# Performance work log

Measured on AMD Instinct MI355X. Metric: run time of the kernel, lower is better.

The kernel has to match this reference:

```python
import jax, jax.numpy as jnp
import numpy as np

BATCH = 65536
VEC = 512       # CLIP embedding dim
K = 1024        # num_cluster
GAMMA = 0.99
EPS = 1e-05


def setup_inputs() -> dict:
    key = jax.random.key(0)
    k1, k2, k3 = jax.random.split(key, 3)
    batch_vectors = jax.random.normal(k1, (BATCH, VEC), dtype=jnp.float32)
    weight = jax.random.normal(k2, (VEC, K), dtype=jnp.float32)        # codebook, stored (vec_size, num_cluster)
    cluster_size = jnp.ones((K,), dtype=jnp.float32)
    embed_avg = jax.random.normal(k3, (VEC, K), dtype=jnp.float32)
    return {
        "batch_vectors": batch_vectors,
        "weight": weight,
        "cluster_size": cluster_size,
        "embed_avg": embed_avg,
    }


def reference(batch_vectors, weight, cluster_size, embed_avg):
    """One minibatch_update step of clusteringEMA_torch.

    Returns the updated codebook `weight` of shape (vec_size, num_cluster).
    """
    gamma = GAMMA
    eps = EPS
    num_cluster = weight.shape[1]

    # nearest centroid: squared L2 distance has the same argmin as the L2 norm
    x2 = jnp.sum(batch_vectors * batch_vectors, axis=1, keepdims=True)   # (B,1)
    w2 = jnp.sum(weight * weight, axis=0)[None, :]                       # (1,K)
    dist2 = x2 + w2 - 2.0 * (batch_vectors @ weight)                     # (B,K)
    argmin = jnp.argmin(dist2, axis=-1)                                  # (B,)

    # per-cluster counts (one-hot sum), zeros replaced by 1
    counts = jnp.zeros((num_cluster,), dtype=batch_vectors.dtype).at[argmin].add(1.0)
    n_idx_choice = jnp.where(counts == 0, 1.0, counts)

    # EMA of cluster sizes
    new_cluster_size = gamma * cluster_size + (1.0 - gamma) * n_idx_choice

    # embed_sum = x^T @ onehot  == per-cluster sum of assigned vectors, (vec,K)
    embed_sum = jax.ops.segment_sum(batch_vectors, argmin, num_segments=num_cluster).T
    new_embed_avg = gamma * embed_avg + (1.0 - gamma) * embed_sum

    # Laplace-smoothed normalization
    n = jnp.sum(new_cluster_size)
    cs = (new_cluster_size + eps) / (n + num_cluster * eps) * n
    new_weight = new_embed_avg / cs[None, :]
    return new_weight
```

## Files before the change

kernel.cpp:

```cpp
#include <hip/hip_runtime.h>

typedef unsigned int uint;
typedef unsigned short ushort_t;
typedef unsigned long long u64;
typedef __attribute__((ext_vector_type(4))) float f32x4;
typedef __attribute__((ext_vector_type(8))) __bf16 bf16x8;
typedef __attribute__((ext_vector_type(8))) unsigned short us8;

#define BATCH 65536
#define VEC 512
#define K 1024
#define GAMMA 0.99f
#define EPS 1e-05f
#define SEG 64
#define MARGIN 0.75f

#define NKT (VEC / 32)

__device__ __forceinline__ ushort_t rtn(float f) {
    uint u = __float_as_uint(f);
    return (ushort_t)((u + 0x7FFFu + ((u >> 16) & 1u)) >> 16);
}

__device__ __forceinline__ void gl16(const void* g, void* l) {
    __builtin_amdgcn_global_load_lds(
        (const __attribute__((address_space(1))) unsigned int*)g,
        (__attribute__((address_space(3))) unsigned int*)l, 16, 0, 0);
}

__device__ __forceinline__ float dec_key(uint e) {
    uint b = (e & 0x80000000u) ? (e & 0x7FFFFFFFu) : ~e;
    return __uint_as_float(b);
}

__global__ void k_pack_w(const float* __restrict__ w, us8* __restrict__ wpk,
                         float* __restrict__ wT, float* __restrict__ w2p,
                         int* __restrict__ cc ) {
    __shared__ float lds[32][257];
    const int g = blockIdx.x;
    const int gx = g >> 4, ks = g & 15;
    const int t = threadIdx.x;

#pragma unroll
    for (int r = 0; r < 32; ++r)
        lds[r][t] = w[(size_t)(ks * 32 + r) * K + gx * 256 + t];
    __syncthreads();

    float s = 0.f;
#pragma unroll
    for (int r = 0; r < 32; ++r) { float f = lds[r][t]; s += f * f; }
    w2p[ks * K + gx * 256 + t] = s;

#pragma unroll
    for (int i = 0; i < 4; ++i) {
        const int o = i * 256 + t;
        const int lane = o & 63, ct = o >> 6;
        const int cl = ct * 16 + (lane & 15);
        const int r0 = (lane >> 4) * 8;
        us8 v;
#pragma unroll
        for (int j = 0; j < 8; ++j) v[j] = rtn(lds[r0 + j][cl]);
        wpk[(size_t)g * 1024 + o] = v;
    }

#pragma unroll
    for (int rr = 0; rr < 8; ++rr) {
        f32x4 v = {lds[rr * 4 + 0][t], lds[rr * 4 + 1][t], lds[rr * 4 + 2][t], lds[rr * 4 + 3][t]};
        *(f32x4*)&wT[(size_t)(gx * 256 + t) * VEC + ks * 32 + rr * 4] = v;
    }

    if (g < 8) cc[g * 256 + t] = 0;
    if (g == 8 && t == 0) cc[2048] = 0;
}

__launch_bounds__(512, 4)
__global__ void k_gemm(const float* __restrict__ x, const us8* __restrict__ wpk,
                       const float* __restrict__ w2p,
                       u64* __restrict__ keysA, u64* __restrict__ keysB) {
    __shared__ us8 a_lds[2][512];
    __shared__ us8 b_lds[2][1024];

    const int blk = blockIdx.x;
    const int gy = (blk & 7) * 64 + ((blk >> 3) >> 2);
    const int gx = (blk >> 3) & 3;
    const int t = threadIdx.x;
    const int lane = t & 63;
    const int wv = t >> 6;
    const int wm = wv >> 2;
    const int wn = wv & 3;

    const us8* bsrc = wpk + (size_t)gx * (NKT * 1024);

    const int al = t & 63;
    const float* xp = x + (size_t)(gy * 128 + (t >> 6) * 16 + (al & 15)) * VEC + (al >> 4) * 8;
    f32x4 av0, av1;
    auto aload = [&](int kt) {
        const float* p = xp + kt * 32;
        av0 = *(const f32x4*)p;
        av1 = *(const f32x4*)(p + 4);
    };
    auto awrite = [&](int buf) {
        us8 h;
#pragma unroll
        for (int j = 0; j < 4; ++j) { h[j] = rtn(av0[j]); h[4 + j] = rtn(av1[j]); }
        a_lds[buf][t] = h;
    };
    auto bstage = [&](int buf, int kt) {
        const us8* sb = bsrc + (size_t)kt * 1024;
        gl16(sb + t, &b_lds[buf][t]);
        gl16(sb + 512 + t, &b_lds[buf][512 + t]);
    };

    f32x4 acc[4][4];
#pragma unroll
    for (int i = 0; i < 4; ++i)
#pragma unroll
        for (int j = 0; j < 4; ++j) acc[i][j] = (f32x4){0.f, 0.f, 0.f, 0.f};

    aload(0);
    bstage(0, 0);
    awrite(0);
    __syncthreads();

    for (int tk = 0; tk < NKT; ++tk) {
        const int buf = tk & 1;
        const bool nx = (tk + 1 < NKT);
        if (nx) {
            aload(tk + 1);
            bstage(buf ^ 1, tk + 1);
        }
        bf16x8 bh[4];
#pragma unroll
        for (int ct = 0; ct < 4; ++ct)
            bh[ct] = __builtin_bit_cast(bf16x8, b_lds[buf][(wn * 4 + ct) * 64 + lane]);
#pragma unroll
        for (int rt = 0; rt < 4; ++rt) {
            bf16x8 ah = __builtin_bit_cast(bf16x8, a_lds[buf][(wm * 4 + rt) * 64 + lane]);
#pragma unroll
            for (int ct = 0; ct < 4; ++ct)
                acc[rt][ct] = __builtin_amdgcn_mfma_f32_16x16x32_bf16(ah, bh[ct], acc[rt][ct], 0, 0, 0);
        }
        if (nx) awrite(buf ^ 1);
        __syncthreads();
    }

    const int col_base = gx * 256 + wn * 64;
    float w2c[4];
#pragma unroll
    for (int ct = 0; ct < 4; ++ct) {
        const int col = col_base + ct * 16 + (lane & 15);
        float s = 0.f;
#pragma unroll
        for (int p = 0; p < 16; ++p) s += w2p[p * K + col];
        w2c[ct] = s;
    }
    const int slot = gx * 4 + wn;

#pragma unroll
    for (int rt = 0; rt < 4; ++rt) {
#pragma unroll
        for (int reg = 0; reg < 4; ++reg) {
            u64 k1 = ~0ull, k2 = ~0ull;
#pragma unroll
            for (int ct = 0; ct < 4; ++ct) {
                float dist = w2c[ct] - 2.0f * acc[rt][ct][reg];
                uint su = __float_as_uint(dist);
                su = (su & 0x80000000u) ? ~su : (su | 0x80000000u);
                const u64 key = ((u64)su << 32) | (uint)(col_base + ct * 16 + (lane & 15));
                if (key < k1) { k2 = k1; k1 = key; }
                else if (key < k2) { k2 = key; }
            }
#pragma unroll
            for (int m = 1; m < 16; m <<= 1) {
                u64 o1 = __shfl_xor((unsigned long long)k1, m);
                u64 o2 = __shfl_xor((unsigned long long)k2, m);
                u64 lo = k1 < o1 ? k1 : o1;
                u64 hi = k1 < o1 ? o1 : k1;
                u64 mn2 = k2 < o2 ? k2 : o2;
                k1 = lo;
                k2 = hi < mn2 ? hi : mn2;
            }
            if ((lane & 15) == 0) {
                const int row = gy * 128 + wm * 64 + rt * 16 + (lane >> 4) * 4 + reg;
                keysA[(size_t)slot * BATCH + row] = k1;
                keysB[(size_t)slot * BATCH + row] = k2;
            }
        }
    }
}

__global__ void k_verify(const u64* __restrict__ keysA, const u64* __restrict__ keysB,
                         int* __restrict__ am, int* __restrict__ counts,
                         u64* __restrict__ list, int* __restrict__ listcnt,
                         float* __restrict__ esum) {
    const int r = blockIdx.x * 256 + threadIdx.x;
    f32x4 z = {0.f, 0.f, 0.f, 0.f};
    ((f32x4*)esum)[r * 2] = z;
    ((f32x4*)esum)[r * 2 + 1] = z;

    u64 m1 = ~0ull, s = ~0ull;
    int i1 = 0;
#pragma unroll
    for (int i = 0; i < 16; ++i) {
        u64 a = keysA[(size_t)i * BATCH + r];
        if (a < m1) { s = m1; m1 = a; i1 = i; }
        else if (a < s) s = a;
    }
    u64 b = keysB[(size_t)i1 * BATCH + r];
    u64 m2 = s < b ? s : b;

    const float d1 = dec_key((uint)(m1 >> 32));
    const float d2 = dec_key((uint)(m2 >> 32));
    const int c1 = (int)(uint)m1 & 1023;
    const int c2 = (int)(uint)m2 & 1023;

    if (d2 - d1 > MARGIN) {
        am[r] = c1;
        atomicAdd(&counts[c1], 1);
    } else {
        int p = atomicAdd(listcnt, 1);
        list[p] = ((u64)(uint)r << 32) | ((uint)c1 << 10) | (uint)c2;
    }
}

__launch_bounds__(256)
__global__ void k_recheck(const float* __restrict__ x, const float* __restrict__ wT,
                          const float* __restrict__ w2p, const u64* __restrict__ list,
                          const int* __restrict__ listcnt, int* __restrict__ am,
                          int* __restrict__ counts) {
    const int gwid = (blockIdx.x * 256 + threadIdx.x) >> 6;
    const int lane = threadIdx.x & 63;
    const int n = *listcnt;
    for (int idx = gwid; idx < n; idx += 1024) {
        const u64 e = list[idx];
        const int r = (int)(e >> 32);
        const int c1 = (int)((e >> 10) & 1023);
        const int c2 = (int)(e & 1023);
        const f32x4 x0 = *(const f32x4*)&x[(size_t)r * VEC + lane * 8];
        const f32x4 x1 = *(const f32x4*)&x[(size_t)r * VEC + lane * 8 + 4];
        float d[2];
        const int cc[2] = {c1, c2};
#pragma unroll
        for (int j = 0; j < 2; ++j) {
            const int c = cc[j];
            const f32x4 w0 = *(const f32x4*)&wT[(size_t)c * VEC + lane * 8];
            const f32x4 w1 = *(const f32x4*)&wT[(size_t)c * VEC + lane * 8 + 4];
            float p = x0[0] * w0[0] + x0[1] * w0[1] + x0[2] * w0[2] + x0[3] * w0[3]
                    + x1[0] * w1[0] + x1[1] * w1[1] + x1[2] * w1[2] + x1[3] * w1[3];
#pragma unroll
            for (int m = 1; m < 64; m <<= 1) p += __shfl_xor(p, m);
            float w2 = 0.f;
#pragma unroll
            for (int q = 0; q < 16; ++q) w2 += w2p[q * K + c];
            d[j] = w2 - 2.0f * p;
        }
        const int win = (d[0] < d[1] || (d[0] == d[1] && c1 < c2)) ? c1 : c2;
        if (lane == 0) {
            am[r] = win;
            atomicAdd(&counts[win], 1);
        }
    }
}

__global__ void k_scan(const int* __restrict__ counts,
                       const float* __restrict__ cluster_size,
                       int* __restrict__ offsets, float* __restrict__ cs) {
    __shared__ int wsum[16];
    __shared__ float fw[16];
    const int t = threadIdx.x;
    const int lane = t & 63, wid = t >> 6;
    const int c = counts[t];

    int s = c;
#pragma unroll
    for (int d = 1; d < 64; d <<= 1) {
        int o = __shfl_up(s, d);
        if (lane >= d) s += o;
    }
    float ncs = GAMMA * cluster_size[t] + (1.0f - GAMMA) * ((c == 0) ? 1.0f : (float)c);
    float fs = ncs;
#pragma unroll
    for (int d = 32; d > 0; d >>= 1) fs += __shfl_xor(fs, d);

    if (lane == 63) wsum[wid] = s;
    if (lane == 0) fw[wid] = fs;
    __syncthreads();
    if (wid == 0 && lane < 16) {
        int v = wsum[lane];
#pragma unroll
        for (int d = 1; d < 16; d <<= 1) {
            int o = __shfl_up(v, d);
            if (lane >= d) v += o;
        }
        wsum[lane] = v;
    }
    __syncthreads();
    const int base = wid ? wsum[wid - 1] : 0;
    offsets[t] = base + s - c;

    float n = 0.f;
#pragma unroll
    for (int i = 0; i < 16; ++i) n += fw[i];
    cs[t] = (ncs + EPS) / (n + (float)K * EPS) * n;
}

__global__ void k_scatter(const int* __restrict__ am, const int* __restrict__ offsets,
                          int* __restrict__ cursor, int* __restrict__ sorted,
                          int* __restrict__ sortedk) {
    const int b = blockIdx.x * blockDim.x + threadIdx.x;
    const int k = am[b];
    const int pos = atomicAdd(&cursor[k], 1);
    sorted[offsets[k] + pos] = b;
    sortedk[offsets[k] + pos] = k;
}

__launch_bounds__(512)
__global__ void k_segred(const float* __restrict__ x, const int* __restrict__ sorted,
                         const int* __restrict__ sortedk, float* __restrict__ esum) {
    __shared__ int srow[SEG];
    __shared__ int skid[SEG];
    const int b = blockIdx.x;
    const int t = threadIdx.x;
    if (t < SEG) {
        srow[t] = sorted[b * SEG + t];
        skid[t] = sortedk[b * SEG + t];
    }
    __syncthreads();

    float a = 0.f;
    int cur = skid[0];
#pragma unroll 8
    for (int i = 0; i < SEG; ++i) {
        const int k = skid[i];
        if (k != cur) {
            atomicAdd(&esum[(size_t)cur * VEC + t], a);
            a = 0.f;
            cur = k;
        }
        a += x[(size_t)srow[i] * VEC + t];
    }
    atomicAdd(&esum[(size_t)cur * VEC + t], a);
}

__launch_bounds__(256)
__global__ void k_finalize(const float* __restrict__ esum, const float* __restrict__ embed_avg,
                           const float* __restrict__ cs, float* __restrict__ out) {
    __shared__ float tile[64][65];
    const int k0 = blockIdx.x * 64;
    const int v0 = blockIdx.y * 64;
    const int c = threadIdx.x & 63;
    const int r0 = threadIdx.x >> 6;
#pragma unroll
    for (int j = 0; j < 16; ++j) {
        const int r = r0 + j * 4;
        tile[r][c] = esum[(size_t)(k0 + r) * VEC + v0 + c];
    }
    __syncthreads();
    const float csk = cs[k0 + c];
#pragma unroll
    for (int j = 0; j < 16; ++j) {
        const int r = r0 + j * 4;
        const size_t o = (size_t)(v0 + r) * K + k0 + c;
        out[o] = (GAMMA * embed_avg[o] + (1.0f - GAMMA) * tile[c][r]) / csk;
    }
}

extern "C" void kernel_launch(void* const* d_in, const int* in_sizes, int n_in,
                              void* d_out, int out_size, void* d_ws, size_t ws_size,
                              hipStream_t stream) {
    const float* x            = (const float*)d_in[0];
    const float* w            = (const float*)d_in[1];
    const float* cluster_size = (const float*)d_in[2];
    const float* embed_avg    = (const float*)d_in[3];
    float* out = (float*)d_out;

    u64*   keysA   = (u64*)d_ws;
    u64*   keysB   = keysA + (size_t)16 * BATCH;
    int*   am      = (int*)(keysB + (size_t)16 * BATCH);
    u64*   list    = (u64*)(am + BATCH);
    float* w2p     = (float*)(list + BATCH);
    float* cs      = w2p + 16 * K;
    int*   cc      = (int*)(cs + K);
    int*   counts  = cc;
    int*   cursor  = cc + K;
    int*   listcnt = cc + 2 * K;
    int*   offsets = cc + 2 * K + 64;
    int*   sorted  = offsets + K;
    int*   sortedk = sorted + BATCH;
    float* esum    = (float*)(sortedk + BATCH);
    us8*   wpk     = (us8*)(esum + (size_t)K * VEC);
    float* wT      = (float*)(wpk + (size_t)64 * 1024);

    k_pack_w<<<64, 256, 0, stream>>>(w, wpk, wT, w2p, cc);
    k_gemm<<<2048, 512, 0, stream>>>(x, wpk, w2p, keysA, keysB);
    k_verify<<<BATCH / 256, 256, 0, stream>>>(keysA, keysB, am, counts, list, listcnt, esum);
    k_recheck<<<256, 256, 0, stream>>>(x, wT, w2p, list, listcnt, am, counts);
    k_scan<<<1, K, 0, stream>>>(counts, cluster_size, offsets, cs);
    k_scatter<<<BATCH / 256, 256, 0, stream>>>(am, offsets, cursor, sorted, sortedk);
    k_segred<<<BATCH / SEG, 512, 0, stream>>>(x, sorted, sortedk, esum);
    k_finalize<<<dim3(K / 64, VEC / 64), 256, 0, stream>>>(esum, embed_avg, cs, out);
}
```

Measured before the change: 388.0 us.

## Enlarge GEMM tile to 256 rows with K-step 64 and vectorize segment reduction

Each GEMM block now covers 256 rows instead of 128 and steps through K in chunks of 64, with each wave holding 8x4 accumulator tiles. This doubles reuse of every B fragment across row tiles and halves the number of barriers and K iterations. The weight packing kernel is reworked to match the new layout, and the partial norm array shrinks to 8 slices. The cost is more registers and LDS per block, lowering occupancy to 2 blocks per CU. The segment reduction now has threads load float4 values over strided rows, which creates more atomic operations per thread.

```diff
diff --git a/kernel.cpp b/kernel.cpp
--- a/kernel.cpp
+++ b/kernel.cpp
@@ -15,7 +15,7 @@
 #define SEG 64
 #define MARGIN 0.75f
 
-#define NKT (VEC / 32)
+#define NKT (VEC / 64)
 
 __device__ __forceinline__ ushort_t rtn(float f) {
     uint u = __float_as_uint(f);
@@ -38,82 +38,95 @@
                          int* __restrict__ cc ) {
     __shared__ float lds[32][257];
     const int g = blockIdx.x;
-    const int gx = g >> 4, ks = g & 15;
+    const int gx = g >> 3, tk = g & 7;
     const int t = threadIdx.x;
 
-#pragma unroll
-    for (int r = 0; r < 32; ++r)
-        lds[r][t] = w[(size_t)(ks * 32 + r) * K + gx * 256 + t];
-    __syncthreads();
-
     float s = 0.f;
 #pragma unroll
-    for (int r = 0; r < 32; ++r) { float f = lds[r][t]; s += f * f; }
-    w2p[ks * K + gx * 256 + t] = s;
-
-#pragma unroll
-    for (int i = 0; i < 4; ++i) {
-        const int o = i * 256 + t;
-        const int lane = o & 63, ct = o >> 6;
-        const int cl = ct * 16 + (lane & 15);
-        const int r0 = (lane >> 4) * 8;
-        us8 v;
-#pragma unroll
-        for (int j = 0; j < 8; ++j) v[j] = rtn(lds[r0 + j][cl]);
-        wpk[(size_t)g * 1024 + o] = v;
-    }
-
-#pragma unroll
-    for (int rr = 0; rr < 8; ++rr) {
-        f32x4 v = {lds[rr * 4 + 0][t], lds[rr * 4 + 1][t], lds[rr * 4 + 2][t], lds[rr * 4 + 3][t]};
-        *(f32x4*)&wT[(size_t)(gx * 256 + t) * VEC + ks * 32 + rr * 4] = v;
-    }
+    for (int ih = 0; ih < 2; ++ih) {
+        __syncthreads();
+#pragma unroll
+        for (int r = 0; r < 32; ++r)
+            lds[r][t] = w[(size_t)(tk * 64 + ih * 32 + r) * K + gx * 256 + t];
+        __syncthreads();
+
+#pragma unroll
+        for (int r = 0; r < 32; ++r) { float f = lds[r][t]; s += f * f; }
+
+#pragma unroll
+        for (int i = 0; i < 4; ++i) {
+            const int c = (i * 256 + t);
+            const int cslab = c >> 6, lane = c & 63;
+            const int cl = cslab * 16 + (lane & 15);
+            const int r0 = (lane >> 4) * 8;
+            us8 v;
+#pragma unroll
+            for (int j = 0; j < 8; ++j) v[j] = rtn(lds[r0 + j][cl]);
+            wpk[(size_t)g * 2048 + cslab * 128 + ih * 64 + lane] = v;
+        }
+
+#pragma unroll
+        for (int rr = 0; rr < 8; ++rr) {
+            f32x4 v = {lds[rr * 4 + 0][t], lds[rr * 4 + 1][t], lds[rr * 4 + 2][t], lds[rr * 4 + 3][t]};
+            *(f32x4*)&wT[(size_t)(gx * 256 + t) * VEC + tk * 64 + ih * 32 + rr * 4] = v;
+        }
+    }
+    w2p[tk * K + gx * 256 + t] = s;
 
     if (g < 8) cc[g * 256 + t] = 0;
     if (g == 8 && t == 0) cc[2048] = 0;
 }
 
-__launch_bounds__(512, 4)
+__launch_bounds__(512, 2)
 __global__ void k_gemm(const float* __restrict__ x, const us8* __restrict__ wpk,
                        const float* __restrict__ w2p,
                        u64* __restrict__ keysA, u64* __restrict__ keysB) {
-    __shared__ us8 a_lds[2][512];
-    __shared__ us8 b_lds[2][1024];
+    __shared__ us8 a_lds[2][2048];
+    __shared__ us8 b_lds[2][2048];
 
     const int blk = blockIdx.x;
-    const int gy = (blk & 7) * 64 + ((blk >> 3) >> 2);
-    const int gx = (blk >> 3) & 3;
+    const int r = blk >> 3;
+    const int gy = (blk & 7) * 32 + (r >> 2);
+    const int gx = r & 3;
     const int t = threadIdx.x;
     const int lane = t & 63;
     const int wv = t >> 6;
     const int wm = wv >> 2;
     const int wn = wv & 3;
 
-    const us8* bsrc = wpk + (size_t)gx * (NKT * 1024);
-
-    const int al = t & 63;
-    const float* xp = x + (size_t)(gy * 128 + (t >> 6) * 16 + (al & 15)) * VEC + (al >> 4) * 8;
-    f32x4 av0, av1;
-    auto aload = [&](int kt) {
-        const float* p = xp + kt * 32;
-        av0 = *(const f32x4*)p;
-        av1 = *(const f32x4*)(p + 4);
+    const us8* bsrc = wpk + (size_t)gx * (NKT * 2048);
+
+    const int ksub_t = (t >> 6) & 1;
+    const int koff = ksub_t * 32 + ((t >> 4) & 3) * 8;
+    f32x4 av[4][2];
+    auto aload = [&](int tk) {
+#pragma unroll
+        for (int i = 0; i < 4; ++i) {
+            const int row = gy * 256 + ((t >> 7) + 4 * i) * 16 + (t & 15);
+            const float* p = x + (size_t)row * VEC + tk * 64 + koff;
+            av[i][0] = *(const f32x4*)p;
+            av[i][1] = *(const f32x4*)(p + 4);
+        }
     };
     auto awrite = [&](int buf) {
-        us8 h;
-#pragma unroll
-        for (int j = 0; j < 4; ++j) { h[j] = rtn(av0[j]); h[4 + j] = rtn(av1[j]); }
-        a_lds[buf][t] = h;
+#pragma unroll
+        for (int i = 0; i < 4; ++i) {
+            us8 h;
+#pragma unroll
+            for (int j = 0; j < 4; ++j) { h[j] = rtn(av[i][0][j]); h[4 + j] = rtn(av[i][1][j]); }
+            a_lds[buf][t + i * 512] = h;
+        }
     };
-    auto bstage = [&](int buf, int kt) {
-        const us8* sb = bsrc + (size_t)kt * 1024;
-        gl16(sb + t, &b_lds[buf][t]);
-        gl16(sb + 512 + t, &b_lds[buf][512 + t]);
+    auto bstage = [&](int buf, int tk) {
+        const us8* sb = bsrc + (size_t)tk * 2048;
+#pragma unroll
+        for (int i = 0; i < 4; ++i)
+            gl16(sb + t + i * 512, &b_lds[buf][t + i * 512]);
     };
 
-    f32x4 acc[4][4];
-#pragma unroll
-    for (int i = 0; i < 4; ++i)
+    f32x4 acc[8][4];
+#pragma unroll
+    for (int i = 0; i < 8; ++i)
 #pragma unroll
         for (int j = 0; j < 4; ++j) acc[i][j] = (f32x4){0.f, 0.f, 0.f, 0.f};
 
@@ -129,16 +142,19 @@
             aload(tk + 1);
             bstage(buf ^ 1, tk + 1);
         }
-        bf16x8 bh[4];
-#pragma unroll
-        for (int ct = 0; ct < 4; ++ct)
-            bh[ct] = __builtin_bit_cast(bf16x8, b_lds[buf][(wn * 4 + ct) * 64 + lane]);
-#pragma unroll
-        for (int rt = 0; rt < 4; ++rt) {
-            bf16x8 ah = __builtin_bit_cast(bf16x8, a_lds[buf][(wm * 4 + rt) * 64 + lane]);
+#pragma unroll
+        for (int ksub = 0; ksub < 2; ++ksub) {
+            bf16x8 bh[4];
 #pragma unroll
             for (int ct = 0; ct < 4; ++ct)
-                acc[rt][ct] = __builtin_amdgcn_mfma_f32_16x16x32_bf16(ah, bh[ct], acc[rt][ct], 0, 0, 0);
+                bh[ct] = __builtin_bit_cast(bf16x8, b_lds[buf][(wn * 4 + ct) * 128 + ksub * 64 + lane]);
+#pragma unroll
+            for (int rt = 0; rt < 8; ++rt) {
+                bf16x8 ah = __builtin_bit_cast(bf16x8, a_lds[buf][(wm * 8 + rt) * 128 + ksub * 64 + lane]);
+#pragma unroll
+                for (int ct = 0; ct < 4; ++ct)
+                    acc[rt][ct] = __builtin_amdgcn_mfma_f32_16x16x32_bf16(ah, bh[ct], acc[rt][ct], 0, 0, 0);
+            }
         }
         if (nx) awrite(buf ^ 1);
         __syncthreads();
@@ -151,13 +167,13 @@
         const int col = col_base + ct * 16 + (lane & 15);
         float s = 0.f;
 #pragma unroll
-        for (int p = 0; p < 16; ++p) s += w2p[p * K + col];
+        for (int p = 0; p < 8; ++p) s += w2p[p * K + col];
         w2c[ct] = s;
     }
     const int slot = gx * 4 + wn;
 
 #pragma unroll
-    for (int rt = 0; rt < 4; ++rt) {
+    for (int rt = 0; rt < 8; ++rt) {
 #pragma unroll
         for (int reg = 0; reg < 4; ++reg) {
             u64 k1 = ~0ull, k2 = ~0ull;
@@ -181,7 +197,7 @@
                 k2 = hi < mn2 ? hi : mn2;
             }
             if ((lane & 15) == 0) {
-                const int row = gy * 128 + wm * 64 + rt * 16 + (lane >> 4) * 4 + reg;
+                const int row = gy * 256 + wm * 128 + rt * 16 + (lane >> 4) * 4 + reg;
                 keysA[(size_t)slot * BATCH + row] = k1;
                 keysB[(size_t)slot * BATCH + row] = k2;
             }
@@ -239,10 +255,10 @@
         const f32x4 x0 = *(const f32x4*)&x[(size_t)r * VEC + lane * 8];
         const f32x4 x1 = *(const f32x4*)&x[(size_t)r * VEC + lane * 8 + 4];
         float d[2];
-        const int cc[2] = {c1, c2};
+        const int cc2[2] = {c1, c2};
 #pragma unroll
         for (int j = 0; j < 2; ++j) {
-            const int c = cc[j];
+            const int c = cc2[j];
             const f32x4 w0 = *(const f32x4*)&wT[(size_t)c * VEC + lane * 8];
             const f32x4 w1 = *(const f32x4*)&wT[(size_t)c * VEC + lane * 8 + 4];
             float p = x0[0] * w0[0] + x0[1] * w0[1] + x0[2] * w0[2] + x0[3] * w0[3]
@@ -251,7 +267,7 @@
             for (int m = 1; m < 64; m <<= 1) p += __shfl_xor(p, m);
             float w2 = 0.f;
 #pragma unroll
-            for (int q = 0; q < 16; ++q) w2 += w2p[q * K + c];
+            for (int q = 0; q < 8; ++q) w2 += w2p[q * K + c];
             d[j] = w2 - 2.0f * p;
         }
         const int win = (d[0] < d[1] || (d[0] == d[1] && c1 < c2)) ? c1 : c2;
@@ -327,19 +343,24 @@
     }
     __syncthreads();
 
-    float a = 0.f;
-    int cur = skid[0];
-#pragma unroll 8
-    for (int i = 0; i < SEG; ++i) {
+    const int rg = t >> 7;
+    const int vq = t & 127;
+    f32x4 a = {0.f, 0.f, 0.f, 0.f};
+    int cur = skid[rg];
+    for (int i = rg; i < SEG; i += 4) {
         const int k = skid[i];
         if (k != cur) {
-            atomicAdd(&esum[(size_t)cur * VEC + t], a);
-            a = 0.f;
+            float* e = &esum[(size_t)cur * VEC + vq * 4];
+            atomicAdd(e + 0, a[0]); atomicAdd(e + 1, a[1]);
+            atomicAdd(e + 2, a[2]); atomicAdd(e + 3, a[3]);
+            a = (f32x4){0.f, 0.f, 0.f, 0.f};
             cur = k;
         }
-        a += x[(size_t)srow[i] * VEC + t];
-    }
-    atomicAdd(&esum[(size_t)cur * VEC + t], a);
+        a += *(const f32x4*)&x[(size_t)srow[i] * VEC + vq * 4];
+    }
+    float* e = &esum[(size_t)cur * VEC + vq * 4];
+    atomicAdd(e + 0, a[0]); atomicAdd(e + 1, a[1]);
+    atomicAdd(e + 2, a[2]); atomicAdd(e + 3, a[3]);
 }
 
 __launch_bounds__(256)
@@ -379,7 +400,7 @@
     int*   am      = (int*)(keysB + (size_t)16 * BATCH);
     u64*   list    = (u64*)(am + BATCH);
     float* w2p     = (float*)(list + BATCH);
-    float* cs      = w2p + 16 * K;
+    float* cs      = w2p + 8 * K;
     int*   cc      = (int*)(cs + K);
     int*   counts  = cc;
     int*   cursor  = cc + K;
@@ -389,10 +410,10 @@
     int*   sortedk = sorted + BATCH;
     float* esum    = (float*)(sortedk + BATCH);
     us8*   wpk     = (us8*)(esum + (size_t)K * VEC);
-    float* wT      = (float*)(wpk + (size_t)64 * 1024);
-
-    k_pack_w<<<64, 256, 0, stream>>>(w, wpk, wT, w2p, cc);
-    k_gemm<<<2048, 512, 0, stream>>>(x, wpk, w2p, keysA, keysB);
+    float* wT      = (float*)(wpk + (size_t)32 * 2048);
+
+    k_pack_w<<<32, 256, 0, stream>>>(w, wpk, wT, w2p, cc);
+    k_gemm<<<1024, 512, 0, stream>>>(x, wpk, w2p, keysA, keysB);
     k_verify<<<BATCH / 256, 256, 0, stream>>>(keysA, keysB, am, counts, list, listcnt, esum);
     k_recheck<<<256, 256, 0, stream>>>(x, wT, w2p, list, listcnt, am, counts);
     k_scan<<<1, K, 0, stream>>>(counts, cluster_size, offsets, cs);
```

New measurement: 510.8 us. 31.6% more time.

## Shrink GEMM column tile to 128 and fuse recheck into verify

Applied to the files above, without the earlier changes.

The distance GEMM now uses 256-thread blocks covering 128 rows by 128 columns, eight column groups instead of four, with each thread loading two A rows. The codebook packing kernel is resized to match. The separate recheck kernel and its global ambiguous-row list are removed: each verify block collects its near-tie rows in shared memory and re-scores them in fp32 right away. This removes one launch and a global atomic counter, but doubles the number of bf16 conversions of the x tile, and the keys layout still writes 16 slots.

```diff
diff --git a/kernel.cpp b/kernel.cpp
--- a/kernel.cpp
+++ b/kernel.cpp
@@ -36,23 +36,28 @@
 __global__ void k_pack_w(const float* __restrict__ w, us8* __restrict__ wpk,
                          float* __restrict__ wT, float* __restrict__ w2p,
                          int* __restrict__ cc ) {
-    __shared__ float lds[32][257];
+    __shared__ float lds[32][129];
     const int g = blockIdx.x;
     const int gx = g >> 4, ks = g & 15;
     const int t = threadIdx.x;
 
 #pragma unroll
-    for (int r = 0; r < 32; ++r)
-        lds[r][t] = w[(size_t)(ks * 32 + r) * K + gx * 256 + t];
-    __syncthreads();
-
-    float s = 0.f;
-#pragma unroll
-    for (int r = 0; r < 32; ++r) { float f = lds[r][t]; s += f * f; }
-    w2p[ks * K + gx * 256 + t] = s;
-
-#pragma unroll
-    for (int i = 0; i < 4; ++i) {
+    for (int i = 0; i < 16; ++i) {
+        const int idx = i * 256 + t;
+        const int row = idx >> 7, col = idx & 127;
+        lds[row][col] = w[(size_t)(ks * 32 + row) * K + gx * 128 + col];
+    }
+    __syncthreads();
+
+    if (t < 128) {
+        float s = 0.f;
+#pragma unroll
+        for (int r = 0; r < 32; ++r) { float f = lds[r][t]; s += f * f; }
+        w2p[ks * K + gx * 128 + t] = s;
+    }
+
+#pragma unroll
+    for (int i = 0; i < 2; ++i) {
         const int o = i * 256 + t;
         const int lane = o & 63, ct = o >> 6;
         const int cl = ct * 16 + (lane & 15);
@@ -60,55 +65,68 @@
         us8 v;
 #pragma unroll
         for (int j = 0; j < 8; ++j) v[j] = rtn(lds[r0 + j][cl]);
-        wpk[(size_t)g * 1024 + o] = v;
-    }
-
-#pragma unroll
-    for (int rr = 0; rr < 8; ++rr) {
-        f32x4 v = {lds[rr * 4 + 0][t], lds[rr * 4 + 1][t], lds[rr * 4 + 2][t], lds[rr * 4 + 3][t]};
-        *(f32x4*)&wT[(size_t)(gx * 256 + t) * VEC + ks * 32 + rr * 4] = v;
+        wpk[(size_t)g * 512 + o] = v;
+    }
+
+    {
+        const int c = t & 127;
+        const int rb = (t >> 7) * 16;
+#pragma unroll
+        for (int rr = 0; rr < 4; ++rr) {
+            f32x4 v = {lds[rb + rr * 4 + 0][c], lds[rb + rr * 4 + 1][c],
+                       lds[rb + rr * 4 + 2][c], lds[rb + rr * 4 + 3][c]};
+            *(f32x4*)&wT[(size_t)(gx * 128 + c) * VEC + ks * 32 + rb + rr * 4] = v;
+        }
     }
 
     if (g < 8) cc[g * 256 + t] = 0;
-    if (g == 8 && t == 0) cc[2048] = 0;
-}
-
-__launch_bounds__(512, 4)
+}
+
+__launch_bounds__(256, 4)
 __global__ void k_gemm(const float* __restrict__ x, const us8* __restrict__ wpk,
                        const float* __restrict__ w2p,
                        u64* __restrict__ keysA, u64* __restrict__ keysB) {
     __shared__ us8 a_lds[2][512];
-    __shared__ us8 b_lds[2][1024];
+    __shared__ us8 b_lds[2][512];
 
     const int blk = blockIdx.x;
-    const int gy = (blk & 7) * 64 + ((blk >> 3) >> 2);
-    const int gx = (blk >> 3) & 3;
+    const int ord = blk >> 3;
+    const int gx = ord & 7;
+    const int gy = (blk & 7) * 64 + (ord >> 3);
     const int t = threadIdx.x;
     const int lane = t & 63;
     const int wv = t >> 6;
-    const int wm = wv >> 2;
-    const int wn = wv & 3;
-
-    const us8* bsrc = wpk + (size_t)gx * (NKT * 1024);
+    const int wm = wv >> 1;
+    const int wn = wv & 1;
+
+    const us8* bsrc = wpk + (size_t)gx * (NKT * 512);
 
     const int al = t & 63;
-    const float* xp = x + (size_t)(gy * 128 + (t >> 6) * 16 + (al & 15)) * VEC + (al >> 4) * 8;
-    f32x4 av0, av1;
+    const float* xp0 = x + (size_t)(gy * 128 + (t >> 6) * 16 + (al & 15)) * VEC + (al >> 4) * 8;
+    const float* xp1 = xp0 + (size_t)64 * VEC;
+    f32x4 av0, av1, av2, av3;
     auto aload = [&](int kt) {
-        const float* p = xp + kt * 32;
-        av0 = *(const f32x4*)p;
-        av1 = *(const f32x4*)(p + 4);
+        const float* p0 = xp0 + kt * 32;
+        av0 = *(const f32x4*)p0;
+        av1 = *(const f32x4*)(p0 + 4);
+        const float* p1 = xp1 + kt * 32;
+        av2 = *(const f32x4*)p1;
+        av3 = *(const f32x4*)(p1 + 4);
     };
     auto awrite = [&](int buf) {
-        us8 h;
-#pragma unroll
-        for (int j = 0; j < 4; ++j) { h[j] = rtn(av0[j]); h[4 + j] = rtn(av1[j]); }
-        a_lds[buf][t] = h;
+        us8 h0, h1;
+#pragma unroll
+        for (int j = 0; j < 4; ++j) {
+            h0[j] = rtn(av0[j]); h0[4 + j] = rtn(av1[j]);
+            h1[j] = rtn(av2[j]); h1[4 + j] = rtn(av3[j]);
+        }
+        a_lds[buf][t] = h0;
+        a_lds[buf][256 + t] = h1;
     };
     auto bstage = [&](int buf, int kt) {
-        const us8* sb = bsrc + (size_t)kt * 1024;
+        const us8* sb = bsrc + (size_t)kt * 512;
         gl16(sb + t, &b_lds[buf][t]);
-        gl16(sb + 512 + t, &b_lds[buf][512 + t]);
+        gl16(sb + 256 + t, &b_lds[buf][256 + t]);
     };
 
     f32x4 acc[4][4];
@@ -144,7 +162,7 @@
         __syncthreads();
     }
 
-    const int col_base = gx * 256 + wn * 64;
+    const int col_base = gx * 128 + wn * 64;
     float w2c[4];
 #pragma unroll
     for (int ct = 0; ct < 4; ++ct) {
@@ -154,7 +172,7 @@
         for (int p = 0; p < 16; ++p) s += w2p[p * K + col];
         w2c[ct] = s;
     }
-    const int slot = gx * 4 + wn;
+    const int slot = gx * 2 + wn;
 
 #pragma unroll
     for (int rt = 0; rt < 4; ++rt) {
@@ -190,10 +208,20 @@
 }
 
 __global__ void k_verify(const u64* __restrict__ keysA, const u64* __restrict__ keysB,
+                         const float* __restrict__ x, const float* __restrict__ wT,
+                         const float* __restrict__ w2p,
                          int* __restrict__ am, int* __restrict__ counts,
-                         u64* __restrict__ list, int* __restrict__ listcnt,
                          float* __restrict__ esum) {
-    const int r = blockIdx.x * 256 + threadIdx.x;
+    __shared__ int lrow[256];
+    __shared__ int lcc[256];
+    __shared__ int lcnt;
+    const int t = threadIdx.x;
+    const int r = blockIdx.x * 256 + t;
+    const int lane = t & 63;
+
+    if (t == 0) lcnt = 0;
+    __syncthreads();
+
     f32x4 z = {0.f, 0.f, 0.f, 0.f};
     ((f32x4*)esum)[r * 2] = z;
     ((f32x4*)esum)[r * 2 + 1] = z;
@@ -218,31 +246,24 @@
         am[r] = c1;
         atomicAdd(&counts[c1], 1);
     } else {
-        int p = atomicAdd(listcnt, 1);
-        list[p] = ((u64)(uint)r << 32) | ((uint)c1 << 10) | (uint)c2;
-    }
-}
-
-__launch_bounds__(256)
-__global__ void k_recheck(const float* __restrict__ x, const float* __restrict__ wT,
-                          const float* __restrict__ w2p, const u64* __restrict__ list,
-                          const int* __restrict__ listcnt, int* __restrict__ am,
-                          int* __restrict__ counts) {
-    const int gwid = (blockIdx.x * 256 + threadIdx.x) >> 6;
-    const int lane = threadIdx.x & 63;
-    const int n = *listcnt;
-    for (int idx = gwid; idx < n; idx += 1024) {
-        const u64 e = list[idx];
-        const int r = (int)(e >> 32);
-        const int c1 = (int)((e >> 10) & 1023);
-        const int c2 = (int)(e & 1023);
-        const f32x4 x0 = *(const f32x4*)&x[(size_t)r * VEC + lane * 8];
-        const f32x4 x1 = *(const f32x4*)&x[(size_t)r * VEC + lane * 8 + 4];
+        int p = atomicAdd(&lcnt, 1);
+        lrow[p] = r;
+        lcc[p] = (c1 << 10) | c2;
+    }
+    __syncthreads();
+
+    const int n = lcnt;
+    for (int idx = t >> 6; idx < n; idx += 4) {
+        const int r2 = lrow[idx];
+        const int cc1 = lcc[idx] >> 10;
+        const int cc2 = lcc[idx] & 1023;
+        const f32x4 x0 = *(const f32x4*)&x[(size_t)r2 * VEC + lane * 8];
+        const f32x4 x1 = *(const f32x4*)&x[(size_t)r2 * VEC + lane * 8 + 4];
         float d[2];
-        const int cc[2] = {c1, c2};
+        const int cand[2] = {cc1, cc2};
 #pragma unroll
         for (int j = 0; j < 2; ++j) {
-            const int c = cc[j];
+            const int c = cand[j];
             const f32x4 w0 = *(const f32x4*)&wT[(size_t)c * VEC + lane * 8];
             const f32x4 w1 = *(const f32x4*)&wT[(size_t)c * VEC + lane * 8 + 4];
             float p = x0[0] * w0[0] + x0[1] * w0[1] + x0[2] * w0[2] + x0[3] * w0[3]
@@ -254,9 +275,9 @@
             for (int q = 0; q < 16; ++q) w2 += w2p[q * K + c];
             d[j] = w2 - 2.0f * p;
         }
-        const int win = (d[0] < d[1] || (d[0] == d[1] && c1 < c2)) ? c1 : c2;
+        const int win = (d[0] < d[1] || (d[0] == d[1] && cc1 < cc2)) ? cc1 : cc2;
         if (lane == 0) {
-            am[r] = win;
+            am[r2] = win;
             atomicAdd(&counts[win], 1);
         }
     }
@@ -377,24 +398,21 @@
     u64*   keysA   = (u64*)d_ws;
     u64*   keysB   = keysA + (size_t)16 * BATCH;
     int*   am      = (int*)(keysB + (size_t)16 * BATCH);
-    u64*   list    = (u64*)(am + BATCH);
-    float* w2p     = (float*)(list + BATCH);
+    float* w2p     = (float*)(am + BATCH);
     float* cs      = w2p + 16 * K;
     int*   cc      = (int*)(cs + K);
     int*   counts  = cc;
     int*   cursor  = cc + K;
-    int*   listcnt = cc + 2 * K;
-    int*   offsets = cc + 2 * K + 64;
+    int*   offsets = cc + 2 * K;
     int*   sorted  = offsets + K;
     int*   sortedk = sorted + BATCH;
     float* esum    = (float*)(sortedk + BATCH);
     us8*   wpk     = (us8*)(esum + (size_t)K * VEC);
-    float* wT      = (float*)(wpk + (size_t)64 * 1024);
-
-    k_pack_w<<<64, 256, 0, stream>>>(w, wpk, wT, w2p, cc);
-    k_gemm<<<2048, 512, 0, stream>>>(x, wpk, w2p, keysA, keysB);
-    k_verify<<<BATCH / 256, 256, 0, stream>>>(keysA, keysB, am, counts, list, listcnt, esum);
-    k_recheck<<<256, 256, 0, stream>>>(x, wT, w2p, list, listcnt, am, counts);
+    float* wT      = (float*)(wpk + (size_t)128 * 512);
+
+    k_pack_w<<<128, 256, 0, stream>>>(w, wpk, wT, w2p, cc);
+    k_gemm<<<4096, 256, 0, stream>>>(x, wpk, w2p, keysA, keysB);
+    k_verify<<<BATCH / 256, 256, 0, stream>>>(keysA, keysB, x, wT, w2p, am, counts, esum);
     k_scan<<<1, K, 0, stream>>>(counts, cluster_size, offsets, cs);
     k_scatter<<<BATCH / 256, 256, 0, stream>>>(am, offsets, cursor, sorted, sortedk);
     k_segred<<<BATCH / SEG, 512, 0, stream>>>(x, sorted, sortedk, esum);
```

Result: slower. 436.1 us (+12.4%).
